# Kernel tuning notes

Hardware: AMD Instinct MI355X
Metric: run time of the kernel (lower is better)

## Reference

```python
import jax, jax.numpy as jnp
import numpy as np


def setup_inputs() -> dict:
    key = jax.random.key(0)
    k1, k2, k3 = jax.random.split(key, 3)
    B, C, H, W = 16, 64, 256, 256
    x = jax.random.normal(k1, (B, C, H, W), dtype=jnp.float32)
    g = jax.random.normal(k2, (B, C, H, W), dtype=jnp.float32)
    gamma = jax.random.normal(k3, (1,), dtype=jnp.float32)
    return {"x": x, "g": g, "gamma": gamma}


def reference(x, g, gamma):
    # x, g: (B, C, H, W); gamma: (1,)
    B, C, H, W = x.shape
    N = H * W
    xq = x.reshape(B, C, N)   # proj_query / proj_value
    gq = g.reshape(B, C, N)

    # channel-channel energy from x: (B, C, C)
    energy = jnp.einsum('bcn,bdn->bcd', xq, xq)
    attention = jax.nn.softmax(energy, axis=-1)

    # channel-channel energy from guide g: (B, C, C)
    energy_guide = jnp.einsum('bcn,bdn->bcd', gq, gq)
    attention_guide = jax.nn.softmax(energy_guide, axis=-1)

    # chained attention: (B, C, C)
    guide_energy = jnp.einsum('bcd,bde->bce', attention, attention_guide)
    guide_energy_new = jnp.max(guide_energy, axis=-1, keepdims=True) - guide_energy
    guide_attention = jax.nn.softmax(guide_energy_new, axis=-1)

    # apply to values and residual
    out = jnp.einsum('bcd,bdn->bcn', guide_attention, xq).reshape(B, C, H, W)
    return gamma[0] * out + x
```

## Files before the change

### kernel.cpp

```cpp
#include <hip/hip_runtime.h>


typedef _Float16 h8 __attribute__((ext_vector_type(8)));
typedef float    f4 __attribute__((ext_vector_type(4)));
typedef __fp16   p2 __attribute__((ext_vector_type(2)));
typedef unsigned long long ull;

#define NB 16
#define NC 64
#define NPIX 65536
#define GRAM_CHUNK 512
#define NCHUNK (NPIX / GRAM_CHUNK)
#define ROW_H 520
#define LDS_H (64 * ROW_H)

#define AP_NPX 256
#define XT_ROW 72

__device__ __forceinline__ unsigned int pk(float a, float b) {
    p2 v = __builtin_amdgcn_cvt_pkrtz(a, b);
    return __builtin_bit_cast(unsigned int, v);
}

__global__ __launch_bounds__(256) void gram_kernel(
    const float* __restrict__ x, const float* __restrict__ g,
    _Float16* __restrict__ part)
{
    __shared__ __align__(16) _Float16 buf[LDS_H];

    const int tid = threadIdx.x;
    const int mtx = blockIdx.z;
    const float* src = (mtx ? g : x)
        + (size_t)blockIdx.y * NC * NPIX + (size_t)blockIdx.x * GRAM_CHUNK;

    const int w    = tid >> 6;
    const int lane = tid & 63;

    #pragma unroll
    for (int rr = 0; rr < 16; ++rr) {
        const int r = w * 16 + rr;
        const float* rp = src + (size_t)r * NPIX + lane * 4;
        f4 va = *(const f4*)(rp);
        f4 vb = *(const f4*)(rp + 256);
        ull ha = (ull)pk(va.x, va.y) | ((ull)pk(va.z, va.w) << 32);
        ull hb = (ull)pk(vb.x, vb.y) | ((ull)pk(vb.z, vb.w) << 32);
        *reinterpret_cast<ull*>(&buf[r * ROW_H + lane * 4])       = ha;
        *reinterpret_cast<ull*>(&buf[r * ROW_H + 256 + lane * 4]) = hb;
    }
    __syncthreads();

    const int l15   = lane & 15;
    const int khalf = lane >> 4;
    const int abase = (w * 16 + l15) * ROW_H;

    f4 acc[4];
    #pragma unroll
    for (int cb = 0; cb < 4; ++cb) acc[cb] = (f4){0.f, 0.f, 0.f, 0.f};

    #pragma unroll
    for (int ks = 0; ks < 16; ++ks) {
        int koff = ks * 32 + khalf * 8;
        h8 a = *reinterpret_cast<const h8*>(&buf[abase + koff]);
        #pragma unroll
        for (int cb = 0; cb < 4; ++cb) {
            h8 bf = *reinterpret_cast<const h8*>(&buf[(cb * 16 + l15) * ROW_H + koff]);
            acc[cb] = __builtin_amdgcn_mfma_f32_16x16x32_f16(a, bf, acc[cb], 0, 0, 0);
        }
    }

    _Float16* po = part + (((size_t)blockIdx.x * NB + blockIdx.y) * 2 + mtx) * 4096;
    #pragma unroll
    for (int cb = 0; cb < 4; ++cb)
        #pragma unroll
        for (int r = 0; r < 4; ++r)
            po[(w * 16 + khalf * 4 + r) * 64 + cb * 16 + l15] = (_Float16)acc[cb][r];
}

__global__ __launch_bounds__(256) void reduce_kernel(
    const _Float16* __restrict__ part, float* __restrict__ ex, float* __restrict__ eg)
{
    const int idx = blockIdx.x * 256 + threadIdx.x;
    const int bm = idx >> 12;
    const int cd = idx & 4095;
    float s = 0.f;
    #pragma unroll 8
    for (int ch = 0; ch < NCHUNK; ++ch)
        s += (float)part[(size_t)ch * (NB * 2 * 4096) + (size_t)bm * 4096 + cd];
    float* dst = (bm & 1) ? eg : ex;
    dst[(bm >> 1) * 4096 + cd] = s;
}

__global__ __launch_bounds__(256) void chain_kernel(
    const float* __restrict__ ex, const float* __restrict__ eg,
    const float* __restrict__ gammap, float* __restrict__ M)
{
    __shared__ float A1[64][68];
    __shared__ float A2[64][68];
    __shared__ float red[64][4];

    const int b = blockIdx.x;
    const int tid = threadIdx.x;

    if (tid < 64) {
        const int c = tid;
        float r[64];
        #pragma unroll
        for (int d = 0; d < 64; ++d) r[d] = ex[b * 4096 + c * 64 + d];
        float mx = r[0];
        #pragma unroll
        for (int d = 1; d < 64; ++d) mx = fmaxf(mx, r[d]);
        float s = 0.f;
        #pragma unroll
        for (int d = 0; d < 64; ++d) { r[d] = expf(r[d] - mx); s += r[d]; }
        float inv = 1.f / s;
        #pragma unroll
        for (int d = 0; d < 64; ++d) A1[c][d] = r[d] * inv;

        #pragma unroll
        for (int d = 0; d < 64; ++d) r[d] = eg[b * 4096 + c * 64 + d];
        mx = r[0];
        #pragma unroll
        for (int d = 1; d < 64; ++d) mx = fmaxf(mx, r[d]);
        s = 0.f;
        #pragma unroll
        for (int d = 0; d < 64; ++d) { r[d] = expf(r[d] - mx); s += r[d]; }
        inv = 1.f / s;
        #pragma unroll
        for (int d = 0; d < 64; ++d) A2[c][d] = r[d] * inv;
    }
    __syncthreads();

    const int c = tid >> 2, sq = tid & 3;
    float ge[16];
    #pragma unroll
    for (int k = 0; k < 16; ++k) ge[k] = 0.f;
    for (int d = 0; d < 64; ++d) {
        float a = A1[c][d];
        const float* row = &A2[d][sq * 16];
        #pragma unroll
        for (int k = 0; k < 16; ++k) ge[k] = fmaf(a, row[k], ge[k]);
    }

    float mx = ge[0];
    #pragma unroll
    for (int k = 1; k < 16; ++k) mx = fmaxf(mx, ge[k]);
    red[c][sq] = mx;
    __syncthreads();
    float gm = fmaxf(fmaxf(red[c][0], red[c][1]), fmaxf(red[c][2], red[c][3]));
    __syncthreads();

    float gen[16];
    #pragma unroll
    for (int k = 0; k < 16; ++k) gen[k] = gm - ge[k];
    float mx2 = gen[0];
    #pragma unroll
    for (int k = 1; k < 16; ++k) mx2 = fmaxf(mx2, gen[k]);
    red[c][sq] = mx2;
    __syncthreads();
    float m2 = fmaxf(fmaxf(red[c][0], red[c][1]), fmaxf(red[c][2], red[c][3]));
    __syncthreads();

    float p[16];
    float s = 0.f;
    #pragma unroll
    for (int k = 0; k < 16; ++k) { p[k] = expf(gen[k] - m2); s += p[k]; }
    red[c][sq] = s;
    __syncthreads();
    float S = red[c][0] + red[c][1] + red[c][2] + red[c][3];

    float gam = gammap[0];
    float invS = 1.f / S;
    #pragma unroll
    for (int k = 0; k < 16; ++k) {
        int e = sq * 16 + k;
        M[b * 4096 + c * 64 + e] = gam * p[k] * invS;
    }
}

__global__ __launch_bounds__(256) void apply_kernel(
    const float* __restrict__ x, const float* __restrict__ M,
    float* __restrict__ out)
{
    __shared__ __align__(16) _Float16 xT[AP_NPX * XT_ROW];
    __shared__ __align__(16) _Float16 Ml[64 * XT_ROW];

    const int tid = threadIdx.x;
    const int b = blockIdx.y;
    const int n0 = blockIdx.x * AP_NPX;
    const float* xb = x + (size_t)b * NC * NPIX + n0;

    #pragma unroll
    for (int it = 0; it < 8; ++it) {
        int e = it * 256 + tid;
        int q  = e & 63;
        int dp = e >> 6;
        f4 va = *(const f4*)(xb + (size_t)(2 * dp)     * NPIX + q * 4);
        f4 vb = *(const f4*)(xb + (size_t)(2 * dp + 1) * NPIX + q * 4);
        #pragma unroll
        for (int j = 0; j < 4; ++j) {
            float aj = (j == 0) ? va.x : (j == 1) ? va.y : (j == 2) ? va.z : va.w;
            float bj = (j == 0) ? vb.x : (j == 1) ? vb.y : (j == 2) ? vb.z : vb.w;
            *reinterpret_cast<unsigned int*>(&xT[(q * 4 + j) * XT_ROW + 2 * dp]) = pk(aj, bj);
        }
    }
    const float* Mb = M + b * 4096;
    #pragma unroll
    for (int it = 0; it < 4; ++it) {
        int e = it * 256 + tid;
        int c  = e >> 4;
        int qq = e & 15;
        f4 mv = *(const f4*)(Mb + c * 64 + qq * 4);
        *reinterpret_cast<unsigned int*>(&Ml[c * XT_ROW + qq * 4])     = pk(mv.x, mv.y);
        *reinterpret_cast<unsigned int*>(&Ml[c * XT_ROW + qq * 4 + 2]) = pk(mv.z, mv.w);
    }
    __syncthreads();

    const int w    = tid >> 6;
    const int lane = tid & 63;
    const int l15  = lane & 15;
    const int kh   = lane >> 4;

    h8 bfrag[4][2];
    #pragma unroll
    for (int nb = 0; nb < 4; ++nb)
        #pragma unroll
        for (int ks = 0; ks < 2; ++ks)
            bfrag[nb][ks] = *reinterpret_cast<const h8*>(
                &xT[(w * 64 + nb * 16 + l15) * XT_ROW + ks * 32 + kh * 8]);

    f4 acc[4][4];
    #pragma unroll
    for (int cb = 0; cb < 4; ++cb)
        #pragma unroll
        for (int nb = 0; nb < 4; ++nb) acc[cb][nb] = (f4){0.f, 0.f, 0.f, 0.f};

    #pragma unroll
    for (int cb = 0; cb < 4; ++cb) {
        #pragma unroll
        for (int ks = 0; ks < 2; ++ks) {
            h8 a = *reinterpret_cast<const h8*>(
                &Ml[(cb * 16 + l15) * XT_ROW + ks * 32 + kh * 8]);
            #pragma unroll
            for (int nb = 0; nb < 4; ++nb)
                acc[cb][nb] = __builtin_amdgcn_mfma_f32_16x16x32_f16(a, bfrag[nb][ks], acc[cb][nb], 0, 0, 0);
        }
    }

    const size_t base = (size_t)b * NC * NPIX + n0 + w * 64;
    #pragma unroll
    for (int cb = 0; cb < 4; ++cb) {
        #pragma unroll
        for (int r = 0; r < 4; ++r) {
            const int row = cb * 16 + kh * 4 + r;
            #pragma unroll
            for (int nb = 0; nb < 4; ++nb) {
                size_t idx = base + (size_t)row * NPIX + nb * 16 + l15;
                out[idx] = acc[cb][nb][r] + x[idx];
            }
        }
    }
}

extern "C" void kernel_launch(void* const* d_in, const int* in_sizes, int n_in,
                              void* d_out, int out_size, void* d_ws, size_t ws_size,
                              hipStream_t stream) {
    const float* x     = (const float*)d_in[0];
    const float* g     = (const float*)d_in[1];
    const float* gamma = (const float*)d_in[2];
    float* out = (float*)d_out;
    float* ws  = (float*)d_ws;

    float* ex = ws;
    float* eg = ws + NB * 4096;
    float* M  = ws + 2 * NB * 4096;

    _Float16* part = (_Float16*)out;

    gram_kernel<<<dim3(NCHUNK, NB, 2), 256, 0, stream>>>(x, g, part);
    reduce_kernel<<<512, 256, 0, stream>>>(part, ex, eg);
    chain_kernel<<<NB, 256, 0, stream>>>(ex, eg, gamma, M);
    apply_kernel<<<dim3(NPIX / AP_NPX, NB), 256, 0, stream>>>(x, M, out);
}
```

Before: 267.3 us.

## Stage fp16 copy of x during Gram pass and read it in apply

The Gram kernel already converts x to fp16 for its MFMA work. It now also writes that fp16 data, in a chunked tile layout, to a workspace buffer. The apply kernel reads this half-width copy instead of re-reading fp32 x, and uses it for both the matmul operand and the residual. This trades an extra 128 MB write in the first pass for a halved read in the last pass. The residual is now added in fp16 precision, and the new path only runs when the workspace is large enough.

```diff
diff --git a/kernel.cpp b/kernel.cpp
--- a/kernel.cpp
+++ b/kernel.cpp
@@ -2,6 +2,7 @@
 
 
 typedef _Float16 h8 __attribute__((ext_vector_type(8)));
+typedef unsigned short u8v __attribute__((ext_vector_type(8)));
 typedef float    f4 __attribute__((ext_vector_type(4)));
 typedef __fp16   p2 __attribute__((ext_vector_type(2)));
 typedef unsigned long long ull;
@@ -24,7 +25,7 @@
 
 __global__ __launch_bounds__(256) void gram_kernel(
     const float* __restrict__ x, const float* __restrict__ g,
-    _Float16* __restrict__ part)
+    _Float16* __restrict__ part, _Float16* __restrict__ xt)
 {
     __shared__ __align__(16) _Float16 buf[LDS_H];
 
@@ -35,6 +36,10 @@
 
     const int w    = tid >> 6;
     const int lane = tid & 63;
+
+    char* tb = nullptr;
+    if (xt && mtx == 0)
+        tb = (char*)(xt + ((size_t)blockIdx.y * NCHUNK + blockIdx.x) * (64 * 512));
 
     #pragma unroll
     for (int rr = 0; rr < 16; ++rr) {
@@ -46,6 +51,10 @@
         ull hb = (ull)pk(vb.x, vb.y) | ((ull)pk(vb.z, vb.w) << 32);
         *reinterpret_cast<ull*>(&buf[r * ROW_H + lane * 4])       = ha;
         *reinterpret_cast<ull*>(&buf[r * ROW_H + 256 + lane * 4]) = hb;
+        if (tb) {
+            *reinterpret_cast<ull*>(tb + r * 1024 + lane * 8)       = ha;
+            *reinterpret_cast<ull*>(tb + r * 1024 + 512 + lane * 8) = hb;
+        }
     }
     __syncthreads();
 
@@ -177,7 +186,94 @@
     }
 }
 
-__global__ __launch_bounds__(256) void apply_kernel(
+__global__ __launch_bounds__(256) void apply_tiled(
+    const _Float16* __restrict__ xt, const float* __restrict__ M,
+    float* __restrict__ out)
+{
+    __shared__ __align__(16) _Float16 xT[AP_NPX * XT_ROW];
+    __shared__ __align__(16) _Float16 Ml[64 * XT_ROW];
+
+    const int tid = threadIdx.x;
+    const int b = blockIdx.y;
+    const int n0 = blockIdx.x * AP_NPX;
+    const int cidx = blockIdx.x >> 1;
+    const int half = blockIdx.x & 1;
+    const _Float16* tile = xt + ((size_t)b * NCHUNK + cidx) * (64 * 512) + half * 256;
+
+    #pragma unroll
+    for (int it = 0; it < 4; ++it) {
+        int e  = it * 256 + tid;
+        int dp = e >> 5;
+        int q8 = e & 31;
+        int nl = q8 * 8;
+        u8v v0 = *(const u8v*)(tile + (size_t)(2 * dp)     * 512 + nl);
+        u8v v1 = *(const u8v*)(tile + (size_t)(2 * dp + 1) * 512 + nl);
+        #pragma unroll
+        for (int j = 0; j < 8; ++j) {
+            unsigned int u = (unsigned int)v0[j] | ((unsigned int)v1[j] << 16);
+            *reinterpret_cast<unsigned int*>(&xT[(nl + j) * XT_ROW + 2 * dp]) = u;
+        }
+    }
+    const float* Mb = M + b * 4096;
+    #pragma unroll
+    for (int it = 0; it < 4; ++it) {
+        int e = it * 256 + tid;
+        int c  = e >> 4;
+        int qq = e & 15;
+        f4 mv = *(const f4*)(Mb + c * 64 + qq * 4);
+        *reinterpret_cast<unsigned int*>(&Ml[c * XT_ROW + qq * 4])     = pk(mv.x, mv.y);
+        *reinterpret_cast<unsigned int*>(&Ml[c * XT_ROW + qq * 4 + 2]) = pk(mv.z, mv.w);
+    }
+    __syncthreads();
+
+    const int w    = tid >> 6;
+    const int lane = tid & 63;
+    const int l15  = lane & 15;
+    const int kh   = lane >> 4;
+
+    h8 bfrag[4][2];
+    #pragma unroll
+    for (int nb = 0; nb < 4; ++nb)
+        #pragma unroll
+        for (int ks = 0; ks < 2; ++ks)
+            bfrag[nb][ks] = *reinterpret_cast<const h8*>(
+                &xT[(w * 64 + nb * 16 + l15) * XT_ROW + ks * 32 + kh * 8]);
+
+    f4 acc[4][4];
+    #pragma unroll
+    for (int cb = 0; cb < 4; ++cb)
+        #pragma unroll
+        for (int nb = 0; nb < 4; ++nb) acc[cb][nb] = (f4){0.f, 0.f, 0.f, 0.f};
+
+    #pragma unroll
+    for (int cb = 0; cb < 4; ++cb) {
+        #pragma unroll
+        for (int ks = 0; ks < 2; ++ks) {
+            h8 a = *reinterpret_cast<const h8*>(
+                &Ml[(cb * 16 + l15) * XT_ROW + ks * 32 + kh * 8]);
+            #pragma unroll
+            for (int nb = 0; nb < 4; ++nb)
+                acc[cb][nb] = __builtin_amdgcn_mfma_f32_16x16x32_f16(a, bfrag[nb][ks], acc[cb][nb], 0, 0, 0);
+        }
+    }
+
+    const size_t base = (size_t)b * NC * NPIX + n0 + w * 64;
+    #pragma unroll
+    for (int cb = 0; cb < 4; ++cb) {
+        #pragma unroll
+        for (int r = 0; r < 4; ++r) {
+            const int row = cb * 16 + kh * 4 + r;
+            #pragma unroll
+            for (int nb = 0; nb < 4; ++nb) {
+                float resid = (float)xT[(w * 64 + nb * 16 + l15) * XT_ROW + row];
+                size_t idx = base + (size_t)row * NPIX + nb * 16 + l15;
+                out[idx] = acc[cb][nb][r] + resid;
+            }
+        }
+    }
+}
+
+__global__ __launch_bounds__(256) void apply_legacy(
     const float* __restrict__ x, const float* __restrict__ M,
     float* __restrict__ out)
 {
@@ -274,10 +370,18 @@
     float* eg = ws + NB * 4096;
     float* M  = ws + 2 * NB * 4096;
 
+    const size_t xt_off_floats = (1u << 20) / 4;
+    const size_t xt_bytes = (size_t)NB * NCHUNK * 64 * 512 * sizeof(_Float16);
+    const bool tiled = ws_size >= ((size_t)(1u << 20) + xt_bytes);
+    _Float16* xt = tiled ? (_Float16*)(ws + xt_off_floats) : nullptr;
+
     _Float16* part = (_Float16*)out;
 
-    gram_kernel<<<dim3(NCHUNK, NB, 2), 256, 0, stream>>>(x, g, part);
+    gram_kernel<<<dim3(NCHUNK, NB, 2), 256, 0, stream>>>(x, g, part, xt);
     reduce_kernel<<<512, 256, 0, stream>>>(part, ex, eg);
     chain_kernel<<<NB, 256, 0, stream>>>(ex, eg, gamma, M);
-    apply_kernel<<<dim3(NPIX / AP_NPX, NB), 256, 0, stream>>>(x, M, out);
-}
+    if (tiled)
+        apply_tiled<<<dim3(NPIX / AP_NPX, NB), 256, 0, stream>>>(xt, M, out);
+    else
+        apply_legacy<<<dim3(NPIX / AP_NPX, NB), 256, 0, stream>>>(x, M, out);
+}
```

After: 272.7 us. 1.02x slower.
